# Kernel tuning notes

Hardware: AMD Instinct MI355X
Metric: run time of the kernel (lower is better)

Reference implementation:

```python
import jax, jax.numpy as jnp
import numpy as np

EPS_NORM = 1e-12  # matches F.normalize eps

def _l2_normalize(x):
    norm = jnp.sqrt(jnp.sum(x * x, axis=-1, keepdims=True))
    return x / jnp.maximum(norm, EPS_NORM)

def setup_inputs() -> dict:
    key = jax.random.key(0)
    k1, k2 = jax.random.split(key)
    N, C, D = 16384, 8192, 1024
    features = jax.random.normal(k1, (N, D), dtype=jnp.float32)
    # prototypes init: normal(mean=const_init=0, std=0.01)
    prototypes = 0.01 * jax.random.normal(k2, (C, D), dtype=jnp.float32)
    distance_scale = jnp.ones((1,), dtype=jnp.float32)
    return {"features": features, "prototypes": prototypes, "distance_scale": distance_scale}

def reference(features, prototypes, distance_scale):
    temperature = 1.0
    f = _l2_normalize(features)      # [N, D]
    p = _l2_normalize(prototypes)    # [C, D]
    # Both rows are unit-norm, so ||f_i - p_j||^2 = 2 - 2 f_i . p_j
    dots = jnp.einsum('nd,cd->nc', f, p)             # [N, C]
    sq = jnp.maximum(2.0 - 2.0 * dots, 1e-12)
    distances = jnp.abs(distance_scale[0]) * jnp.sqrt(sq)
    logits = -distances
    return logits / temperature
```

## Files before the change

kernel.cpp:

```cpp
#include <hip/hip_runtime.h>
#include <hip/hip_bf16.h>
#include <stdint.h>

using bf16x8 = __attribute__((ext_vector_type(8))) short;
using f32x4  = __attribute__((ext_vector_type(4))) float;

#define SBAR()   __builtin_amdgcn_s_barrier()
#define SCHED0() __builtin_amdgcn_sched_barrier(0)
#define LGKM0()  asm volatile("s_waitcnt lgkmcnt(0)" ::: "memory")
#define VMW(n)   asm volatile("s_waitcnt vmcnt(" #n ")" ::: "memory")

__device__ __forceinline__ void gload_lds16(const void* g, void* l) {
  __builtin_amdgcn_global_load_lds(
      (const __attribute__((address_space(1))) void*)g,
      (__attribute__((address_space(3))) void*)l,
      16, 0, 0);
}

__device__ __forceinline__ short f2bf(float f) {
  union { float f; uint32_t u; } c; c.f = f;
  uint32_t u = c.u;
  uint32_t r = (u + 0x7fffu + ((u >> 16) & 1u)) >> 16;
  return (short)(r & 0xffffu);
}

__global__ __launch_bounds__(256) void norm_rows(
    const float* __restrict__ F, const float* __restrict__ P,
    short* __restrict__ Fb, short* __restrict__ Pb, int nF) {
  int row = blockIdx.x;
  const float* src; short* dst;
  if (row < nF) {
    src = F + (size_t)row * 1024; dst = Fb + (size_t)row * 1024;
  } else {
    int r = row - nF;
    src = P + (size_t)r * 1024; dst = Pb + (size_t)r * 1024;
  }
  int tid = threadIdx.x;
  float4 v = ((const float4*)src)[tid];
  float ss = v.x * v.x + v.y * v.y + v.z * v.z + v.w * v.w;
  #pragma unroll
  for (int off = 32; off >= 1; off >>= 1) ss += __shfl_xor(ss, off);
  __shared__ float wsum[4];
  if ((tid & 63) == 0) wsum[tid >> 6] = ss;
  __syncthreads();
  float tot = wsum[0] + wsum[1] + wsum[2] + wsum[3];
  float inv = 1.0f / fmaxf(sqrtf(tot), 1e-12f);
  short4 o;
  o.x = f2bf(v.x * inv); o.y = f2bf(v.y * inv);
  o.z = f2bf(v.z * inv); o.w = f2bf(v.w * inv);
  ((short4*)dst)[tid] = o;
}

#define BM 256
#define BN 256
#define BK 64

__global__ __launch_bounds__(512, 2) void gemm_epi(
    const short* __restrict__ A,
    const short* __restrict__ B,
    const float* __restrict__ scale,
    float* __restrict__ Out, int M, int Cc, int K) {
  __shared__ __align__(16) char smem[2 * 65536];

  const int tid  = threadIdx.x;
  const int wave = tid >> 6;
  const int lane = tid & 63;
  const int wm = wave >> 2;
  const int wn = wave & 3;
  const int hb = wn >> 1;
  const int rbB = (wn & 1) * 4;

  const int nwg = gridDim.x;
  const int cpx = nwg >> 3;
  const int swz = (blockIdx.x & 7) * cpx + (blockIdx.x >> 3);
  const int ntn = Cc / BN;
  const int tm = swz / ntn, tn = swz % ntn;

  const size_t Kb = (size_t)K * 2;
  const char* Ag = (const char*)A + (size_t)tm * BM * Kb;
  const char* Bg = (const char*)B + (size_t)tn * BN * Kb;

  int r0, c0, r1, c1;
  { int s = tid * 16;        int st = s >> 10, w = s & 1023;
    w ^= ((w >> 9) & 1) << 5; r0 = ((st >> 1) << 4) + (w >> 6); c0 = ((st & 1) << 6) + (w & 63); }
  { int s = 8192 + tid * 16; int st = s >> 10, w = s & 1023;
    w ^= ((w >> 9) & 1) << 5; r1 = ((st >> 1) << 4) + (w >> 6); c1 = ((st & 1) << 6) + (w & 63); }

  const int fr  = lane & 15;
  const int fk2 = ((lane >> 4) * 8) * 2;
  const int fragoff = fr * 64 + (fk2 ^ ((fr & 8) ? 32 : 0));

  const char* smA = smem + wm * 16384;
  const char* smB = smem + 32768 + hb * 16384;

  f32x4 acc[8][4];
  #pragma unroll
  for (int i = 0; i < 8; ++i)
    #pragma unroll
    for (int j = 0; j < 4; ++j) acc[i][j] = (f32x4){0.f, 0.f, 0.f, 0.f};

  #define STG_BLO(t, buf) do { const size_t kb = (size_t)(t) * (BK * 2);       \
    char* db = smem + (buf) * 65536 + wave * 1024;                             \
    gload_lds16(Bg + (size_t)(      r0) * Kb + kb + c0, db + 32768);           \
    gload_lds16(Bg + (size_t)(      r1) * Kb + kb + c1, db + 40960); } while (0)
  #define STG_BHI(t, buf) do { const size_t kb = (size_t)(t) * (BK * 2);       \
    char* db = smem + (buf) * 65536 + wave * 1024;                             \
    gload_lds16(Bg + (size_t)(128 + r0) * Kb + kb + c0, db + 49152);           \
    gload_lds16(Bg + (size_t)(128 + r1) * Kb + kb + c1, db + 57344); } while (0)
  #define STG_AEV(t, buf) do { const size_t kb = (size_t)(t) * (BK * 2);       \
    char* db = smem + (buf) * 65536 + wave * 1024;                             \
    gload_lds16(Ag + (size_t)(      r0) * Kb + kb + c0, db);                   \
    gload_lds16(Ag + (size_t)(128 + r0) * Kb + kb + c0, db + 16384); } while (0)
  #define STG_AOD(t, buf) do { const size_t kb = (size_t)(t) * (BK * 2);       \
    char* db = smem + (buf) * 65536 + wave * 1024;                             \
    gload_lds16(Ag + (size_t)(      r1) * Kb + kb + c1, db + 8192);            \
    gload_lds16(Ag + (size_t)(128 + r1) * Kb + kb + c1, db + 24576); } while (0)

  #define LDA(buf, mi, ks) (*(const bf16x8*)(smA + (buf) * 65536 + ((mi) * 2 + (ks)) * 1024 + fragoff))
  #define LDB(buf, nj, ks) (*(const bf16x8*)(smB + (buf) * 65536 + ((rbB + (nj)) * 2 + (ks)) * 1024 + fragoff))

  #define RD_A(AR, buf, mbase)                                                 \
    _Pragma("unroll")                                                          \
    for (int mi = 0; mi < 4; ++mi) {                                           \
      AR[mi][0] = LDA(buf, (mbase) + mi, 0);                                   \
      AR[mi][1] = LDA(buf, (mbase) + mi, 1); }
  #define RD_B(BR, buf, nbase)                                                 \
    _Pragma("unroll")                                                          \
    for (int nj = 0; nj < 2; ++nj) {                                           \
      BR[nj][0] = LDB(buf, (nbase) + nj, 0);                                   \
      BR[nj][1] = LDB(buf, (nbase) + nj, 1); }
  #define MFMA_Q(mbase, nbase, AR, BR)                                         \
    _Pragma("unroll")                                                          \
    for (int mi = 0; mi < 4; ++mi)                                             \
      _Pragma("unroll")                                                        \
      for (int nj = 0; nj < 2; ++nj) {                                         \
        acc[(mbase)+mi][(nbase)+nj] = __builtin_amdgcn_mfma_f32_16x16x32_bf16( \
            AR[mi][0], BR[nj][0], acc[(mbase)+mi][(nbase)+nj], 0, 0, 0);       \
        acc[(mbase)+mi][(nbase)+nj] = __builtin_amdgcn_mfma_f32_16x16x32_bf16( \
            AR[mi][1], BR[nj][1], acc[(mbase)+mi][(nbase)+nj], 0, 0, 0); }

  const int ni = K / (2 * BK);

  STG_BLO(0, 0); STG_BHI(0, 0); STG_AEV(0, 0); STG_AOD(0, 0); SCHED0();
  VMW(2); SCHED0(); SBAR(); SCHED0();

  for (int i = 0; i < ni; ++i) {
    const int t1 = 2 * i + 1;
    const int t2 = 2 * i + 2;
    const bool last = (i == ni - 1);

    bf16x8 a03[4][2], a47[4][2], bA[2][2], bB[2][2];

    RD_A(a03, 0, 0); RD_B(bA, 0, 0);
    STG_BLO(t1, 1); SCHED0();
    SBAR(); LGKM0(); SCHED0();
    __builtin_amdgcn_s_setprio(1); MFMA_Q(0, 0, a03, bA) __builtin_amdgcn_s_setprio(0);
    SBAR(); SCHED0();

    RD_B(bB, 0, 2);
    STG_BHI(t1, 1); SCHED0();
    SBAR(); LGKM0(); SCHED0();
    __builtin_amdgcn_s_setprio(1); MFMA_Q(0, 2, a03, bB) __builtin_amdgcn_s_setprio(0);
    VMW(4); SCHED0();
    SBAR(); SCHED0();

    RD_A(a47, 0, 4);
    STG_AEV(t1, 1); SCHED0();
    SBAR(); LGKM0(); SCHED0();
    __builtin_amdgcn_s_setprio(1); MFMA_Q(4, 2, a47, bB) __builtin_amdgcn_s_setprio(0);
    SBAR(); SCHED0();

    RD_B(bA, 0, 0);
    STG_AOD(t1, 1); SCHED0();
    SBAR(); LGKM0(); SCHED0();
    __builtin_amdgcn_s_setprio(1); MFMA_Q(4, 0, a47, bA) __builtin_amdgcn_s_setprio(0);
    VMW(2); SCHED0();
    SBAR(); SCHED0();

    RD_A(a03, 1, 0); RD_B(bA, 1, 0);
    if (!last) { STG_BLO(t2, 0); } SCHED0();
    SBAR(); LGKM0(); SCHED0();
    __builtin_amdgcn_s_setprio(1); MFMA_Q(0, 0, a03, bA) __builtin_amdgcn_s_setprio(0);
    SBAR(); SCHED0();

    RD_B(bB, 1, 2);
    if (!last) { STG_BHI(t2, 0); } SCHED0();
    SBAR(); LGKM0(); SCHED0();
    __builtin_amdgcn_s_setprio(1); MFMA_Q(0, 2, a03, bB) __builtin_amdgcn_s_setprio(0);
    if (!last) { VMW(4); } else { VMW(0); }
    SCHED0();
    SBAR(); SCHED0();

    RD_A(a47, 1, 4);
    if (!last) { STG_AEV(t2, 0); } SCHED0();
    SBAR(); LGKM0(); SCHED0();
    __builtin_amdgcn_s_setprio(1); MFMA_Q(4, 2, a47, bB) __builtin_amdgcn_s_setprio(0);
    SBAR(); SCHED0();

    RD_B(bA, 1, 0);
    if (!last) { STG_AOD(t2, 0); } SCHED0();
    SBAR(); LGKM0(); SCHED0();
    __builtin_amdgcn_s_setprio(1); MFMA_Q(4, 0, a47, bA) __builtin_amdgcn_s_setprio(0);
    VMW(2); SCHED0();
    SBAR(); SCHED0();
  }

  const float sc = fabsf(scale[0]);
  const int orow0 = tm * BM + wm * 128 + (lane >> 4) * 4;
  const int ocol0 = tn * BN + wn * 64 + fr;
  #pragma unroll
  for (int mi = 0; mi < 8; ++mi) {
    #pragma unroll
    for (int nj = 0; nj < 4; ++nj) {
      const int col = ocol0 + nj * 16;
      #pragma unroll
      for (int r = 0; r < 4; ++r) {
        float d  = acc[mi][nj][r];
        float sq = fmaxf(2.0f - 2.0f * d, 1e-12f);
        __builtin_nontemporal_store(-sc * sqrtf(sq),
            &Out[(size_t)(orow0 + mi * 16 + r) * Cc + col]);
      }
    }
  }
}

extern "C" void kernel_launch(void* const* d_in, const int* in_sizes, int n_in,
                              void* d_out, int out_size, void* d_ws, size_t ws_size,
                              hipStream_t stream) {
  const float* F = (const float*)d_in[0];
  const float* P = (const float*)d_in[1];
  const float* S = (const float*)d_in[2];
  float* Out = (float*)d_out;

  const int D = 1024;
  const int N = in_sizes[0] / D;
  const int C = in_sizes[1] / D;

  short* Fb = (short*)d_ws;
  short* Pb = Fb + (size_t)N * D;

  norm_rows<<<N + C, 256, 0, stream>>>(F, P, Fb, Pb, N);

  dim3 grid((N / BM) * (C / BN));
  gemm_epi<<<grid, 512, 0, stream>>>(Fb, Pb, S, Out, N, C, D);
}
```

Before: 820.8 us.

## Use wave-per-row normalization, 4x4 supertile swizzle, drop sched barriers and nontemporal stores

The normalize kernel now gives each wave its own row and reduces with shuffles only, which removes the LDS reduction and the block barrier. The GEMM tile mapping becomes a hard-coded supertile swizzle that groups tiles in 4x4 blocks per XCD to improve L2 reuse. All sched_barrier fences are removed so the compiler can interleave instructions freely. Output stores change from nontemporal to ordinary stores. The swizzle assumes the exact 64x32 tile grid, and without the fences the compiler may reorder instructions across the hand-built pipeline.

```diff
diff --git a/kernel.cpp b/kernel.cpp
--- a/kernel.cpp
+++ b/kernel.cpp
@@ -6,7 +6,6 @@
 using f32x4  = __attribute__((ext_vector_type(4))) float;
 
 #define SBAR()   __builtin_amdgcn_s_barrier()
-#define SCHED0() __builtin_amdgcn_sched_barrier(0)
 #define LGKM0()  asm volatile("s_waitcnt lgkmcnt(0)" ::: "memory")
 #define VMW(n)   asm volatile("s_waitcnt vmcnt(" #n ")" ::: "memory")
 
@@ -27,7 +26,8 @@
 __global__ __launch_bounds__(256) void norm_rows(
     const float* __restrict__ F, const float* __restrict__ P,
     short* __restrict__ Fb, short* __restrict__ Pb, int nF) {
-  int row = blockIdx.x;
+  const int row  = blockIdx.x * 4 + (threadIdx.x >> 6);
+  const int lane = threadIdx.x & 63;
   const float* src; short* dst;
   if (row < nF) {
     src = F + (size_t)row * 1024; dst = Fb + (size_t)row * 1024;
@@ -35,20 +35,25 @@
     int r = row - nF;
     src = P + (size_t)r * 1024; dst = Pb + (size_t)r * 1024;
   }
-  int tid = threadIdx.x;
-  float4 v = ((const float4*)src)[tid];
-  float ss = v.x * v.x + v.y * v.y + v.z * v.z + v.w * v.w;
+  const float4* s4 = (const float4*)src;
+  float4 v0 = s4[lane], v1 = s4[lane + 64], v2 = s4[lane + 128], v3 = s4[lane + 192];
+  float ss = v0.x*v0.x + v0.y*v0.y + v0.z*v0.z + v0.w*v0.w
+           + v1.x*v1.x + v1.y*v1.y + v1.z*v1.z + v1.w*v1.w
+           + v2.x*v2.x + v2.y*v2.y + v2.z*v2.z + v2.w*v2.w
+           + v3.x*v3.x + v3.y*v3.y + v3.z*v3.z + v3.w*v3.w;
   #pragma unroll
   for (int off = 32; off >= 1; off >>= 1) ss += __shfl_xor(ss, off);
-  __shared__ float wsum[4];
-  if ((tid & 63) == 0) wsum[tid >> 6] = ss;
-  __syncthreads();
-  float tot = wsum[0] + wsum[1] + wsum[2] + wsum[3];
-  float inv = 1.0f / fmaxf(sqrtf(tot), 1e-12f);
+  const float inv = 1.0f / fmaxf(sqrtf(ss), 1e-12f);
+  short4* d4 = (short4*)dst;
   short4 o;
-  o.x = f2bf(v.x * inv); o.y = f2bf(v.y * inv);
-  o.z = f2bf(v.z * inv); o.w = f2bf(v.w * inv);
-  ((short4*)dst)[tid] = o;
+  o.x = f2bf(v0.x*inv); o.y = f2bf(v0.y*inv); o.z = f2bf(v0.z*inv); o.w = f2bf(v0.w*inv);
+  d4[lane] = o;
+  o.x = f2bf(v1.x*inv); o.y = f2bf(v1.y*inv); o.z = f2bf(v1.z*inv); o.w = f2bf(v1.w*inv);
+  d4[lane + 64] = o;
+  o.x = f2bf(v2.x*inv); o.y = f2bf(v2.y*inv); o.z = f2bf(v2.z*inv); o.w = f2bf(v2.w*inv);
+  d4[lane + 128] = o;
+  o.x = f2bf(v3.x*inv); o.y = f2bf(v3.y*inv); o.z = f2bf(v3.z*inv); o.w = f2bf(v3.w*inv);
+  d4[lane + 192] = o;
 }
 
 #define BM 256
@@ -70,21 +75,22 @@
   const int hb = wn >> 1;
   const int rbB = (wn & 1) * 4;
 
-  const int nwg = gridDim.x;
-  const int cpx = nwg >> 3;
-  const int swz = (blockIdx.x & 7) * cpx + (blockIdx.x >> 3);
-  const int ntn = Cc / BN;
-  const int tm = swz / ntn, tn = swz % ntn;
+  const int x  = blockIdx.x & 7;
+  const int c  = blockIdx.x >> 3;
+  const int st = c >> 4, wi = c & 15;
+  const int stm = st >> 3, stn = st & 7;
+  const int tm = x * 8 + stm * 4 + (wi >> 2);
+  const int tn = stn * 4 + (wi & 3);
 
   const size_t Kb = (size_t)K * 2;
   const char* Ag = (const char*)A + (size_t)tm * BM * Kb;
   const char* Bg = (const char*)B + (size_t)tn * BN * Kb;
 
   int r0, c0, r1, c1;
-  { int s = tid * 16;        int st = s >> 10, w = s & 1023;
-    w ^= ((w >> 9) & 1) << 5; r0 = ((st >> 1) << 4) + (w >> 6); c0 = ((st & 1) << 6) + (w & 63); }
-  { int s = 8192 + tid * 16; int st = s >> 10, w = s & 1023;
-    w ^= ((w >> 9) & 1) << 5; r1 = ((st >> 1) << 4) + (w >> 6); c1 = ((st & 1) << 6) + (w & 63); }
+  { int s = tid * 16;        int stq = s >> 10, w = s & 1023;
+    w ^= ((w >> 9) & 1) << 5; r0 = ((stq >> 1) << 4) + (w >> 6); c0 = ((stq & 1) << 6) + (w & 63); }
+  { int s = 8192 + tid * 16; int stq = s >> 10, w = s & 1023;
+    w ^= ((w >> 9) & 1) << 5; r1 = ((stq >> 1) << 4) + (w >> 6); c1 = ((stq & 1) << 6) + (w & 63); }
 
   const int fr  = lane & 15;
   const int fk2 = ((lane >> 4) * 8) * 2;
@@ -141,8 +147,8 @@
 
   const int ni = K / (2 * BK);
 
-  STG_BLO(0, 0); STG_BHI(0, 0); STG_AEV(0, 0); STG_AOD(0, 0); SCHED0();
-  VMW(2); SCHED0(); SBAR(); SCHED0();
+  STG_BLO(0, 0); STG_BHI(0, 0); STG_AEV(0, 0); STG_AOD(0, 0);
+  VMW(2); SBAR();
 
   for (int i = 0; i < ni; ++i) {
     const int t1 = 2 * i + 1;
@@ -152,57 +158,56 @@
     bf16x8 a03[4][2], a47[4][2], bA[2][2], bB[2][2];
 
     RD_A(a03, 0, 0); RD_B(bA, 0, 0);
-    STG_BLO(t1, 1); SCHED0();
-    SBAR(); LGKM0(); SCHED0();
+    STG_BLO(t1, 1);
+    SBAR(); LGKM0();
     __builtin_amdgcn_s_setprio(1); MFMA_Q(0, 0, a03, bA) __builtin_amdgcn_s_setprio(0);
-    SBAR(); SCHED0();
+    SBAR();
 
     RD_B(bB, 0, 2);
-    STG_BHI(t1, 1); SCHED0();
-    SBAR(); LGKM0(); SCHED0();
+    STG_BHI(t1, 1);
+    SBAR(); LGKM0();
     __builtin_amdgcn_s_setprio(1); MFMA_Q(0, 2, a03, bB) __builtin_amdgcn_s_setprio(0);
-    VMW(4); SCHED0();
-    SBAR(); SCHED0();
+    VMW(4);
+    SBAR();
 
     RD_A(a47, 0, 4);
-    STG_AEV(t1, 1); SCHED0();
-    SBAR(); LGKM0(); SCHED0();
+    STG_AEV(t1, 1);
+    SBAR(); LGKM0();
     __builtin_amdgcn_s_setprio(1); MFMA_Q(4, 2, a47, bB) __builtin_amdgcn_s_setprio(0);
-    SBAR(); SCHED0();
+    SBAR();
 
     RD_B(bA, 0, 0);
-    STG_AOD(t1, 1); SCHED0();
-    SBAR(); LGKM0(); SCHED0();
+    STG_AOD(t1, 1);
+    SBAR(); LGKM0();
     __builtin_amdgcn_s_setprio(1); MFMA_Q(4, 0, a47, bA) __builtin_amdgcn_s_setprio(0);
-    VMW(2); SCHED0();
-    SBAR(); SCHED0();
+    VMW(2);
+    SBAR();
 
     RD_A(a03, 1, 0); RD_B(bA, 1, 0);
-    if (!last) { STG_BLO(t2, 0); } SCHED0();
-    SBAR(); LGKM0(); SCHED0();
+    if (!last) { STG_BLO(t2, 0); }
+    SBAR(); LGKM0();
     __builtin_amdgcn_s_setprio(1); MFMA_Q(0, 0, a03, bA) __builtin_amdgcn_s_setprio(0);
-    SBAR(); SCHED0();
+    SBAR();
 
     RD_B(bB, 1, 2);
-    if (!last) { STG_BHI(t2, 0); } SCHED0();
-    SBAR(); LGKM0(); SCHED0();
+    if (!last) { STG_BHI(t2, 0); }
+    SBAR(); LGKM0();
     __builtin_amdgcn_s_setprio(1); MFMA_Q(0, 2, a03, bB) __builtin_amdgcn_s_setprio(0);
     if (!last) { VMW(4); } else { VMW(0); }
-    SCHED0();
-    SBAR(); SCHED0();
+    SBAR();
 
     RD_A(a47, 1, 4);
-    if (!last) { STG_AEV(t2, 0); } SCHED0();
-    SBAR(); LGKM0(); SCHED0();
+    if (!last) { STG_AEV(t2, 0); }
+    SBAR(); LGKM0();
     __builtin_amdgcn_s_setprio(1); MFMA_Q(4, 2, a47, bB) __builtin_amdgcn_s_setprio(0);
-    SBAR(); SCHED0();
+    SBAR();
 
     RD_B(bA, 1, 0);
-    if (!last) { STG_AOD(t2, 0); } SCHED0();
-    SBAR(); LGKM0(); SCHED0();
+    if (!last) { STG_AOD(t2, 0); }
+    SBAR(); LGKM0();
     __builtin_amdgcn_s_setprio(1); MFMA_Q(4, 0, a47, bA) __builtin_amdgcn_s_setprio(0);
-    VMW(2); SCHED0();
-    SBAR(); SCHED0();
+    VMW(2);
+    SBAR();
   }
 
   const float sc = fabsf(scale[0]);
@@ -217,8 +222,7 @@
       for (int r = 0; r < 4; ++r) {
         float d  = acc[mi][nj][r];
         float sq = fmaxf(2.0f - 2.0f * d, 1e-12f);
-        __builtin_nontemporal_store(-sc * sqrtf(sq),
-            &Out[(size_t)(orow0 + mi * 16 + r) * Cc + col]);
+        Out[(size_t)(orow0 + mi * 16 + r) * Cc + col] = -sc * sqrtf(sq);
       }
     }
   }
@@ -239,7 +243,7 @@
   short* Fb = (short*)d_ws;
   short* Pb = Fb + (size_t)N * D;
 
-  norm_rows<<<N + C, 256, 0, stream>>>(F, P, Fb, Pb, N);
+  norm_rows<<<(N + C) / 4, 256, 0, stream>>>(F, P, Fb, Pb, N);
 
   dim3 grid((N / BM) * (C / BN));
   gemm_epi<<<grid, 512, 0, stream>>>(Fb, Pb, S, Out, N, C, D);
```

Result: no change. 807.8 us (-1.6%).
